# Kernel optimization log

Measured on AMD Instinct MI355X. Metric: run time of the kernel, lower is better.

## Reference

```python
import jax, jax.numpy as jnp
import numpy as np

B, T, E = 2, 2048, 768
H = 12
HD = E // H          # 64
ROT = 32             # rotary dim (= head_dim // 2 in CLVP)
SCALE = HD ** -0.5


def rotate_half(x):
    # split last dim into (2, d/2), rotate second half by 90 deg
    x = x.reshape(*x.shape[:-1], 2, x.shape[-1] // 2)
    x1, x2 = x[..., 0, :], x[..., 1, :]
    return jnp.concatenate([-x2, x1], axis=-1)


def apply_rotary_pos_emb(state, freqs):
    # state: (B*H, T, HD); freqs: (1, T, ROT)
    pos_emb_len = freqs.shape[-1]
    s_l, s_r = state[..., :pos_emb_len], state[..., pos_emb_len:]
    f = freqs[:, :, -s_l.shape[-1]:]
    s_l = s_l * jnp.cos(f) + rotate_half(s_l) * jnp.sin(f)
    return jnp.concatenate([s_l, s_r], axis=-1)


def setup_inputs() -> dict:
    key = jax.random.key(0)
    ks = jax.random.split(key, 6)
    hidden_states = jax.random.normal(ks[0], (B, T, E), dtype=jnp.float32)
    rotary_pos_emb = jax.random.uniform(ks[1], (1, T, ROT), dtype=jnp.float32)
    Wq = jax.random.normal(ks[2], (E, E), dtype=jnp.float32) * 0.02
    Wk = jax.random.normal(ks[3], (E, E), dtype=jnp.float32) * 0.02
    Wv = jax.random.normal(ks[4], (E, E), dtype=jnp.float32) * 0.02
    Wo = jax.random.normal(ks[5], (E, E), dtype=jnp.float32) * 0.02
    bo = jnp.zeros((E,), dtype=jnp.float32)
    return {"hidden_states": hidden_states, "rotary_pos_emb": rotary_pos_emb,
            "Wq": Wq, "Wk": Wk, "Wv": Wv, "Wo": Wo, "bo": bo}


def _shape(x):
    # (B, T, E) -> (B*H, T, HD)
    return x.reshape(B, T, H, HD).transpose(0, 2, 1, 3).reshape(B * H, T, HD)


def reference(hidden_states, rotary_pos_emb, Wq, Wk, Wv, Wo, bo):
    # nn.Linear: x @ W.T
    q = _shape(hidden_states @ Wq.T * SCALE)
    k = _shape(hidden_states @ Wk.T)
    v = _shape(hidden_states @ Wv.T)

    q = apply_rotary_pos_emb(q, rotary_pos_emb)
    k = apply_rotary_pos_emb(k, rotary_pos_emb)
    v = apply_rotary_pos_emb(v, rotary_pos_emb)  # CLVP applies RoPE to V too

    attn = jax.nn.softmax(jnp.einsum('bqd,bkd->bqk', q, k), axis=-1)  # (B*H, T, T)
    out = jnp.einsum('bqk,bkd->bqd', attn, v)                          # (B*H, T, HD)
    out = out.reshape(B, H, T, HD).transpose(0, 2, 1, 3).reshape(B, T, E)
    return out @ Wo.T + bo
```

## Files before the change

### kernel.cpp

```cpp
#include <hip/hip_runtime.h>
#include <hip/hip_bf16.h>

typedef unsigned short ushort_t;
typedef __attribute__((ext_vector_type(8))) short short8;
typedef __attribute__((ext_vector_type(4))) float f32x4;

constexpr int B  = 2;
constexpr int T  = 2048;
constexpr int E  = 768;
constexpr int H  = 12;
constexpr int HD = 64;
constexpr float QSCALE = 0.125f;

__device__ __forceinline__ ushort_t f2bf(float x) {
  unsigned int u = __float_as_uint(x);
  u += 0x7fffu + ((u >> 16) & 1u);
  return (ushort_t)(u >> 16);
}

__device__ __forceinline__ unsigned int pack_bf2(float a, float b) {
  __hip_bfloat162 h = __float22bfloat162_rn(float2{a, b});
  return *(unsigned int*)&h;
}

__device__ __forceinline__ int swz(int row, int col) {
  return row * 64 + ((((col >> 3) ^ (row & 7)) << 3) | (col & 7));
}

__device__ __forceinline__ void gl_lds16(const ushort_t* g, ushort_t* l) {
  __builtin_amdgcn_global_load_lds(
      (const __attribute__((address_space(1))) unsigned int*)g,
      (__attribute__((address_space(3))) unsigned int*)l, 16, 0, 0);
}

__global__ __launch_bounds__(256) void cvt_all(
    const float* __restrict__ X,  const float* __restrict__ Wq,
    const float* __restrict__ Wk, const float* __restrict__ Wv,
    const float* __restrict__ Wo, const float* __restrict__ rope,
    ushort_t* __restrict__ Xb,  ushort_t* __restrict__ Wqb,
    ushort_t* __restrict__ Wkb, ushort_t* __restrict__ Wvb,
    ushort_t* __restrict__ Wob, float* __restrict__ ct, float* __restrict__ st)
{
  constexpr int NX4 = (B * T * E) / 4;
  constexpr int NW4 = (E * E) / 4;
  constexpr int NC4 = NX4 + 4 * NW4;
  int i = blockIdx.x * 256 + threadIdx.x;
  if (i < NC4) {
    const float* s; ushort_t* d; int j;
    if (i < NX4) { s = X; d = Xb; j = i; }
    else {
      int t = i - NX4;
      int w = t / NW4; j = t - w * NW4;
      s = (w == 0) ? Wq : (w == 1) ? Wk : (w == 2) ? Wv : Wo;
      d = (w == 0) ? Wqb : (w == 1) ? Wkb : (w == 2) ? Wvb : Wob;
    }
    float4 v = ((const float4*)s)[j];
    ushort4 o;
    o.x = f2bf(v.x); o.y = f2bf(v.y); o.z = f2bf(v.z); o.w = f2bf(v.w);
    ((ushort4*)d)[j] = o;
  } else {
    int j = (i - NC4) * 4;
    float4 f = *(const float4*)(rope + j);
    float c, s;
    sincosf(f.x, &s, &c); ct[j+0] = c; st[j+0] = s;
    sincosf(f.y, &s, &c); ct[j+1] = c; st[j+1] = s;
    sincosf(f.z, &s, &c); ct[j+2] = c; st[j+2] = s;
    sincosf(f.w, &s, &c); ct[j+3] = c; st[j+3] = s;
  }
}

__global__ __launch_bounds__(256) void qkv_gemm(
    const ushort_t* __restrict__ Xb,
    const ushort_t* __restrict__ Wqb, const ushort_t* __restrict__ Wkb,
    const ushort_t* __restrict__ Wvb,
    const float* __restrict__ ct, const float* __restrict__ st,
    ushort_t* __restrict__ qfb, ushort_t* __restrict__ kfb, ushort_t* __restrict__ vfb)
{
  __shared__ __align__(16) ushort_t smem[128 * 64 + 3 * 64 * 64];
  ushort_t* Xs = smem;
  ushort_t* Ws[3] = { smem + 8192, smem + 8192 + 4096, smem + 8192 + 8192 };
  const int tid  = threadIdx.x;
  const int wave = tid >> 6;
  const int lane = tid & 63;
  const int l15  = lane & 15, quad = lane >> 4;
  const int h  = blockIdx.x;
  const int n0 = h * 64;
  const int m0 = blockIdx.y * 128;
  const ushort_t* Wsrc[3] = { Wqb, Wkb, Wvb };

  f32x4 acc[3][2][4];
  #pragma unroll
  for (int z = 0; z < 3; ++z)
    #pragma unroll
    for (int i = 0; i < 2; ++i)
      #pragma unroll
      for (int j = 0; j < 4; ++j) acc[z][i][j] = (f32x4){0.f, 0.f, 0.f, 0.f};

  const int li8 = lane >> 3, lc8 = lane & 7;
  const ushort_t* gX[4]; ushort_t* lX[4];
  #pragma unroll
  for (int j = 0; j < 4; ++j) {
    int row = wave * 32 + j * 8 + li8;
    int c = lc8 ^ (row & 7);
    gX[j] = Xb + (size_t)(m0 + row) * E + c * 8;
    lX[j] = Xs + (wave * 32 + j * 8) * 64;
  }
  const ushort_t* gW[3][2]; ushort_t* lW[3][2];
  #pragma unroll
  for (int z = 0; z < 3; ++z)
    #pragma unroll
    for (int j = 0; j < 2; ++j) {
      int row = wave * 16 + j * 8 + li8;
      int c = lc8 ^ (row & 7);
      gW[z][j] = Wsrc[z] + (size_t)(n0 + row) * E + c * 8;
      lW[z][j] = Ws[z] + (wave * 16 + j * 8) * 64;
    }

  for (int k0 = 0; k0 < E; k0 += 64) {
    #pragma unroll
    for (int j = 0; j < 4; ++j) gl_lds16(gX[j] + k0, lX[j]);
    #pragma unroll
    for (int z = 0; z < 3; ++z)
      #pragma unroll
      for (int j = 0; j < 2; ++j) gl_lds16(gW[z][j] + k0, lW[z][j]);
    __syncthreads();
    short8 a[2][2];
    #pragma unroll
    for (int mt = 0; mt < 2; ++mt)
      #pragma unroll
      for (int kh = 0; kh < 2; ++kh)
        a[mt][kh] = *(const short8*)&Xs[swz(wave * 32 + mt * 16 + l15, kh * 32 + quad * 8)];
    #pragma unroll
    for (int z = 0; z < 3; ++z)
      #pragma unroll
      for (int nt = 0; nt < 4; ++nt)
        #pragma unroll
        for (int kh = 0; kh < 2; ++kh) {
          short8 bb = *(const short8*)&Ws[z][swz(nt * 16 + l15, kh * 32 + quad * 8)];
          #pragma unroll
          for (int mt = 0; mt < 2; ++mt)
            acc[z][mt][nt] = __builtin_amdgcn_mfma_f32_16x16x32_bf16(a[mt][kh], bb, acc[z][mt][nt], 0, 0, 0);
        }
    __syncthreads();
  }

  const int b  = m0 >> 11;
  const int t0 = m0 & (T - 1);
  const int bh = b * H + h;

  #pragma unroll
  for (int z = 0; z < 2; ++z) {
    const float sc = (z == 0) ? QSCALE : 1.0f;
    #pragma unroll
    for (int mt = 0; mt < 2; ++mt) {
      #pragma unroll
      for (int r = 0; r < 4; ++r) {
        int mloc = wave * 32 + mt * 16 + quad * 4 + r;
        int t = (m0 + mloc) & (T - 1);
        float s0 = acc[z][mt][0][r] * sc;
        float s1 = acc[z][mt][1][r] * sc;
        float c0v = ct[t * 32 + l15],      sn0 = st[t * 32 + l15];
        float c1v = ct[t * 32 + 16 + l15], sn1 = st[t * 32 + 16 + l15];
        smem[swz(mloc, l15)]      = f2bf(s0 * c0v - s1 * sn0);
        smem[swz(mloc, 16 + l15)] = f2bf(s1 * c1v + s0 * sn1);
        smem[swz(mloc, 32 + l15)] = f2bf(acc[z][mt][2][r] * sc);
        smem[swz(mloc, 48 + l15)] = f2bf(acc[z][mt][3][r] * sc);
      }
    }
    __syncthreads();
    if (z == 0) {
      #pragma unroll
      for (int i = 0; i < 4; ++i) {
        int p = tid + 256 * i;
        int qtl = p >> 7, kh = (p >> 6) & 1, ln = p & 63;
        int tl = qtl * 16 + (ln & 15);
        int d  = kh * 32 + (ln >> 4) * 8;
        uint4 v = *(const uint4*)&smem[swz(tl, d)];
        size_t off = ((size_t)((bh * 128 + (t0 >> 4) + qtl) * 2 + kh)) * 512 + ln * 8;
        *(uint4*)(qfb + off) = v;
      }
    } else {
      #pragma unroll
      for (int i = 0; i < 4; ++i) {
        int p = tid + 256 * i;
        int ktl = p >> 9, mt = (p >> 7) & 3, kh = (p >> 6) & 1, ln = p & 63;
        int tl = ktl * 64 + mt * 16 + (ln & 15);
        int d  = kh * 32 + (ln >> 4) * 8;
        uint4 v = *(const uint4*)&smem[swz(tl, d)];
        size_t off = ((size_t)(((bh * 32 + (t0 >> 6) + ktl) * 4 + mt) * 2 + kh)) * 512 + ln * 8;
        *(uint4*)(kfb + off) = v;
      }
    }
    __syncthreads();
  }

  #pragma unroll
  for (int mt = 0; mt < 2; ++mt) {
    #pragma unroll
    for (int r = 0; r < 4; ++r) {
      int mloc = wave * 32 + mt * 16 + quad * 4 + r;
      int t = (m0 + mloc) & (T - 1);
      float s0 = acc[2][mt][0][r], s1 = acc[2][mt][1][r];
      float c0v = ct[t * 32 + l15],      sn0 = st[t * 32 + l15];
      float c1v = ct[t * 32 + 16 + l15], sn1 = st[t * 32 + 16 + l15];
      smem[(l15)      * 132 + mloc] = f2bf(s0 * c0v - s1 * sn0);
      smem[(16 + l15) * 132 + mloc] = f2bf(s1 * c1v + s0 * sn1);
      smem[(32 + l15) * 132 + mloc] = f2bf(acc[2][mt][2][r]);
      smem[(48 + l15) * 132 + mloc] = f2bf(acc[2][mt][3][r]);
    }
  }
  __syncthreads();
  #pragma unroll
  for (int i = 0; i < 4; ++i) {
    int p = tid + 256 * i;
    int ktl = p >> 9, nt = (p >> 7) & 3, kh = (p >> 6) & 1, ln = p & 63;
    int d  = nt * 16 + (ln & 15);
    int tl = ktl * 64 + kh * 32 + (ln >> 4) * 8;
    uint4 v = *(const uint4*)&smem[d * 132 + tl];
    size_t off = ((size_t)(((bh * 32 + (t0 >> 6) + ktl) * 4 + nt) * 2 + kh)) * 512 + ln * 8;
    *(uint4*)(vfb + off) = v;
  }
}

__global__ __launch_bounds__(256) void attn_kernel(
    const ushort_t* __restrict__ qfb, const ushort_t* __restrict__ kfb,
    const ushort_t* __restrict__ vfb, ushort_t* __restrict__ cbuf)
{
  __shared__ __align__(16) ushort_t Ps[4][32 * 40];
  __shared__ __align__(16) float Osh[2][32][66];
  __shared__ float Lsh[2][32];
  const int tid  = threadIdx.x;
  const int wave = tid >> 6;
  const int wq = wave >> 1, wk = wave & 1;
  const int lane = tid & 63;
  const int l15  = lane & 15, quad = lane >> 4;
  const int q0 = blockIdx.x * 64;
  const int bh = blockIdx.y;
  const ushort_t* Qf = qfb + (size_t)bh * (T * HD);
  const ushort_t* Kf = kfb + (size_t)bh * (T * HD);
  const ushort_t* Vf = vfb + (size_t)bh * (T * HD);
  ushort_t* Pw = &Ps[wave][0];

  short8 qa[2][2];
  #pragma unroll
  for (int qg = 0; qg < 2; ++qg)
    #pragma unroll
    for (int kh = 0; kh < 2; ++kh)
      qa[qg][kh] = *(const short8*)(Qf + ((size_t)(((q0 >> 4) + wq * 2 + qg) * 2 + kh)) * 512 + lane * 8);

  short8 ka[2][2], va[4];
  #pragma unroll
  for (int i = 0; i < 2; ++i)
    #pragma unroll
    for (int kh = 0; kh < 2; ++kh)
      ka[i][kh] = *(const short8*)(Kf + ((size_t)((wk * 2 + i) * 2 + kh)) * 512 + lane * 8);
  #pragma unroll
  for (int nt = 0; nt < 4; ++nt)
    va[nt] = *(const short8*)(Vf + ((size_t)(nt * 2 + wk)) * 512 + lane * 8);

  f32x4 o[2][4];
  #pragma unroll
  for (int qg = 0; qg < 2; ++qg)
    #pragma unroll
    for (int nt = 0; nt < 4; ++nt) o[qg][nt] = (f32x4){0.f, 0.f, 0.f, 0.f};
  float lsum[2] = {0.f, 0.f};

  for (int kt = 0; kt < T / 64; ++kt) {
    const int ktn = (kt + 1 < T / 64) ? kt + 1 : kt;
    short8 kn[2][2], vn[4];
    #pragma unroll
    for (int i = 0; i < 2; ++i)
      #pragma unroll
      for (int kh = 0; kh < 2; ++kh)
        kn[i][kh] = *(const short8*)(Kf + ((size_t)((ktn * 4 + wk * 2 + i) * 2 + kh)) * 512 + lane * 8);
    #pragma unroll
    for (int nt = 0; nt < 4; ++nt)
      vn[nt] = *(const short8*)(Vf + ((size_t)((ktn * 4 + nt) * 2 + wk)) * 512 + lane * 8);

    f32x4 ss[2][2];
    #pragma unroll
    for (int mt = 0; mt < 2; ++mt)
      #pragma unroll
      for (int qg = 0; qg < 2; ++qg) {
        ss[mt][qg] = (f32x4){0.f, 0.f, 0.f, 0.f};
        ss[mt][qg] = __builtin_amdgcn_mfma_f32_16x16x32_bf16(ka[mt][0], qa[qg][0], ss[mt][qg], 0, 0, 0);
        ss[mt][qg] = __builtin_amdgcn_mfma_f32_16x16x32_bf16(ka[mt][1], qa[qg][1], ss[mt][qg], 0, 0, 0);
      }

    #pragma unroll
    for (int qg = 0; qg < 2; ++qg) {
      #pragma unroll
      for (int mt = 0; mt < 2; ++mt) {
        float p0 = __expf(ss[mt][qg][0]);
        float p1 = __expf(ss[mt][qg][1]);
        float p2 = __expf(ss[mt][qg][2]);
        float p3 = __expf(ss[mt][qg][3]);
        lsum[qg] += (p0 + p1) + (p2 + p3);
        uint2 w2;
        w2.x = pack_bf2(p0, p1);
        w2.y = pack_bf2(p2, p3);
        *(uint2*)&Pw[(qg * 16 + l15) * 40 + mt * 16 + quad * 4] = w2;
      }
    }

    short8 pa0 = *(const short8*)&Pw[(l15) * 40 + quad * 8];
    short8 pa1 = *(const short8*)&Pw[(16 + l15) * 40 + quad * 8];
    #pragma unroll
    for (int nt = 0; nt < 4; ++nt) {
      o[0][nt] = __builtin_amdgcn_mfma_f32_16x16x32_bf16(pa0, va[nt], o[0][nt], 0, 0, 0);
      o[1][nt] = __builtin_amdgcn_mfma_f32_16x16x32_bf16(pa1, va[nt], o[1][nt], 0, 0, 0);
    }

    #pragma unroll
    for (int i = 0; i < 2; ++i) {
      ka[i][0] = kn[i][0];
      ka[i][1] = kn[i][1];
    }
    #pragma unroll
    for (int nt = 0; nt < 4; ++nt) va[nt] = vn[nt];
  }

  #pragma unroll
  for (int qg = 0; qg < 2; ++qg) {
    lsum[qg] += __shfl_xor(lsum[qg], 16);
    lsum[qg] += __shfl_xor(lsum[qg], 32);
  }

  if (wk == 0) {
    #pragma unroll
    for (int qg = 0; qg < 2; ++qg)
      #pragma unroll
      for (int nt = 0; nt < 4; ++nt)
        #pragma unroll
        for (int r = 0; r < 4; ++r)
          Osh[wq][qg * 16 + quad * 4 + r][nt * 16 + l15] = o[qg][nt][r];
    if (lane < 16) {
      Lsh[wq][l15]      = lsum[0];
      Lsh[wq][16 + l15] = lsum[1];
    }
  }
  __syncthreads();
  if (wk == 1) {
    const int b = bh / H, h = bh % H;
    #pragma unroll
    for (int qg = 0; qg < 2; ++qg) {
      float ltot = lsum[qg] + Lsh[wq][qg * 16 + l15];
      float inv0 = 1.0f / ltot;
      #pragma unroll
      for (int r = 0; r < 4; ++r) {
        float inv = __shfl(inv0, quad * 4 + r);
        int t = q0 + wq * 32 + qg * 16 + quad * 4 + r;
        size_t base = ((size_t)b * T + t) * E + h * HD;
        #pragma unroll
        for (int nt = 0; nt < 4; ++nt) {
          float v = o[qg][nt][r] + Osh[wq][qg * 16 + quad * 4 + r][nt * 16 + l15];
          cbuf[base + nt * 16 + l15] = f2bf(v * inv);
        }
      }
    }
  }
}

__global__ __launch_bounds__(256) void out_gemm(
    const ushort_t* __restrict__ Xc, const ushort_t* __restrict__ Wob,
    const float* __restrict__ bo, float* __restrict__ out)
{
  __shared__ __align__(16) ushort_t Xs[128 * 64];
  __shared__ __align__(16) ushort_t Ws[64 * 64];
  const int tid  = threadIdx.x;
  const int wave = tid >> 6;
  const int lane = tid & 63;
  const int l15  = lane & 15, quad = lane >> 4;
  const int n0 = blockIdx.x * 64;
  const int m0 = blockIdx.y * 128;

  f32x4 acc[2][4];
  #pragma unroll
  for (int i = 0; i < 2; ++i)
    #pragma unroll
    for (int j = 0; j < 4; ++j) acc[i][j] = (f32x4){0.f, 0.f, 0.f, 0.f};

  const int li8 = lane >> 3, lc8 = lane & 7;
  const ushort_t* gX[4]; ushort_t* lX[4];
  #pragma unroll
  for (int j = 0; j < 4; ++j) {
    int row = wave * 32 + j * 8 + li8;
    int c = lc8 ^ (row & 7);
    gX[j] = Xc + (size_t)(m0 + row) * E + c * 8;
    lX[j] = Xs + (wave * 32 + j * 8) * 64;
  }
  const ushort_t* gW[2]; ushort_t* lW[2];
  #pragma unroll
  for (int j = 0; j < 2; ++j) {
    int row = wave * 16 + j * 8 + li8;
    int c = lc8 ^ (row & 7);
    gW[j] = Wob + (size_t)(n0 + row) * E + c * 8;
    lW[j] = Ws + (wave * 16 + j * 8) * 64;
  }

  for (int k0 = 0; k0 < E; k0 += 64) {
    #pragma unroll
    for (int j = 0; j < 4; ++j) gl_lds16(gX[j] + k0, lX[j]);
    #pragma unroll
    for (int j = 0; j < 2; ++j) gl_lds16(gW[j] + k0, lW[j]);
    __syncthreads();
    short8 a[2][2];
    #pragma unroll
    for (int mt = 0; mt < 2; ++mt)
      #pragma unroll
      for (int kh = 0; kh < 2; ++kh)
        a[mt][kh] = *(const short8*)&Xs[swz(wave * 32 + mt * 16 + l15, kh * 32 + quad * 8)];
    #pragma unroll
    for (int nt = 0; nt < 4; ++nt) {
      #pragma unroll
      for (int kh = 0; kh < 2; ++kh) {
        short8 bb = *(const short8*)&Ws[swz(nt * 16 + l15, kh * 32 + quad * 8)];
        #pragma unroll
        for (int mt = 0; mt < 2; ++mt)
          acc[mt][nt] = __builtin_amdgcn_mfma_f32_16x16x32_bf16(a[mt][kh], bb, acc[mt][nt], 0, 0, 0);
      }
    }
    __syncthreads();
  }

  float bias[4];
  #pragma unroll
  for (int nt = 0; nt < 4; ++nt) bias[nt] = bo[n0 + nt * 16 + l15];
  #pragma unroll
  for (int mt = 0; mt < 2; ++mt) {
    #pragma unroll
    for (int r = 0; r < 4; ++r) {
      int m = m0 + wave * 32 + mt * 16 + quad * 4 + r;
      float* op = out + (size_t)m * E + n0;
      op[l15]      = acc[mt][0][r] + bias[0];
      op[16 + l15] = acc[mt][1][r] + bias[1];
      op[32 + l15] = acc[mt][2][r] + bias[2];
      op[48 + l15] = acc[mt][3][r] + bias[3];
    }
  }
}

extern "C" void kernel_launch(void* const* d_in, const int* in_sizes, int n_in,
                              void* d_out, int out_size, void* d_ws, size_t ws_size,
                              hipStream_t stream) {
  (void)in_sizes; (void)n_in; (void)out_size; (void)ws_size;
  const float* X    = (const float*)d_in[0];
  const float* rope = (const float*)d_in[1];
  const float* Wq   = (const float*)d_in[2];
  const float* Wk   = (const float*)d_in[3];
  const float* Wv   = (const float*)d_in[4];
  const float* Wo   = (const float*)d_in[5];
  const float* bo   = (const float*)d_in[6];
  float* out = (float*)d_out;

  const size_t NX = (size_t)B * T * E;
  const size_t NW = (size_t)E * E;
  const size_t NR = (size_t)T * 32;
  ushort_t* Xb  = (ushort_t*)d_ws;
  ushort_t* Wqb = Xb  + NX;
  ushort_t* Wkb = Wqb + NW;
  ushort_t* Wvb = Wkb + NW;
  ushort_t* Wob = Wvb + NW;
  ushort_t* qfb = Wob + NW;
  ushort_t* kfb = qfb + NX;
  ushort_t* vfb = kfb + NX;
  ushort_t* cb  = vfb + NX;
  float* ct = (float*)(cb + NX);
  float* st = ct + NR;

  const int total4 = (int)((NX + 4 * NW + NR) / 4);
  cvt_all<<<total4 / 256, 256, 0, stream>>>(X, Wq, Wk, Wv, Wo, rope,
                                            Xb, Wqb, Wkb, Wvb, Wob, ct, st);

  qkv_gemm<<<dim3(H, (B * T) / 128), 256, 0, stream>>>(
      Xb, Wqb, Wkb, Wvb, ct, st, qfb, kfb, vfb);
  attn_kernel<<<dim3(T / 64, B * H), 256, 0, stream>>>(qfb, kfb, vfb, cb);
  out_gemm<<<dim3(E / 64, (B * T) / 128), 256, 0, stream>>>(cb, Wob, bo, out);
}
```

Baseline: 162.6 us.

## Double-buffer LDS in projection GEMMs and compute softmax row sums via MFMA

The QKV and output GEMMs now use two LDS buffers and issue the next k-tile's global-to-LDS loads before computing on the current tile, removing one barrier per iteration so load latency can overlap with MFMA work. The attention kernel drops per-element scalar row-sum accumulation and the shuffle reduction, and instead multiplies the P tile by a ones vector with an extra MFMA per query group. Doubling LDS may reduce occupancy. The async loads into the next buffer rely on the trailing barrier plus the compiler's vmcnt waiting before the next read, which is a correctness risk.

Result: faster. 158.3 us (-2.7%).

```diff
diff --git a/kernel.cpp b/kernel.cpp
--- a/kernel.cpp
+++ b/kernel.cpp
@@ -76,9 +76,7 @@
     const float* __restrict__ ct, const float* __restrict__ st,
     ushort_t* __restrict__ qfb, ushort_t* __restrict__ kfb, ushort_t* __restrict__ vfb)
 {
-  __shared__ __align__(16) ushort_t smem[128 * 64 + 3 * 64 * 64];
-  ushort_t* Xs = smem;
-  ushort_t* Ws[3] = { smem + 8192, smem + 8192 + 4096, smem + 8192 + 8192 };
+  __shared__ __align__(16) ushort_t smem[2 * 20480];
   const int tid  = threadIdx.x;
   const int wave = tid >> 6;
   const int lane = tid & 63;
@@ -97,15 +95,15 @@
       for (int j = 0; j < 4; ++j) acc[z][i][j] = (f32x4){0.f, 0.f, 0.f, 0.f};
 
   const int li8 = lane >> 3, lc8 = lane & 7;
-  const ushort_t* gX[4]; ushort_t* lX[4];
+  const ushort_t* gX[4]; int lXo[4];
   #pragma unroll
   for (int j = 0; j < 4; ++j) {
     int row = wave * 32 + j * 8 + li8;
     int c = lc8 ^ (row & 7);
     gX[j] = Xb + (size_t)(m0 + row) * E + c * 8;
-    lX[j] = Xs + (wave * 32 + j * 8) * 64;
-  }
-  const ushort_t* gW[3][2]; ushort_t* lW[3][2];
+    lXo[j] = (wave * 32 + j * 8) * 64;
+  }
+  const ushort_t* gW[3][2]; int lWo[3][2];
   #pragma unroll
   for (int z = 0; z < 3; ++z)
     #pragma unroll
@@ -113,17 +111,29 @@
       int row = wave * 16 + j * 8 + li8;
       int c = lc8 ^ (row & 7);
       gW[z][j] = Wsrc[z] + (size_t)(n0 + row) * E + c * 8;
-      lW[z][j] = Ws[z] + (wave * 16 + j * 8) * 64;
-    }
+      lWo[z][j] = 8192 + z * 4096 + (wave * 16 + j * 8) * 64;
+    }
+
+  #pragma unroll
+  for (int j = 0; j < 4; ++j) gl_lds16(gX[j], smem + lXo[j]);
+  #pragma unroll
+  for (int z = 0; z < 3; ++z)
+    #pragma unroll
+    for (int j = 0; j < 2; ++j) gl_lds16(gW[z][j], smem + lWo[z][j]);
+  __syncthreads();
 
   for (int k0 = 0; k0 < E; k0 += 64) {
-    #pragma unroll
-    for (int j = 0; j < 4; ++j) gl_lds16(gX[j] + k0, lX[j]);
-    #pragma unroll
-    for (int z = 0; z < 3; ++z)
-      #pragma unroll
-      for (int j = 0; j < 2; ++j) gl_lds16(gW[z][j] + k0, lW[z][j]);
-    __syncthreads();
+    const int cur = (k0 >> 6) & 1;
+    const int nxt = cur ^ 1;
+    if (k0 + 64 < E) {
+      #pragma unroll
+      for (int j = 0; j < 4; ++j) gl_lds16(gX[j] + k0 + 64, smem + nxt * 20480 + lXo[j]);
+      #pragma unroll
+      for (int z = 0; z < 3; ++z)
+        #pragma unroll
+        for (int j = 0; j < 2; ++j) gl_lds16(gW[z][j] + k0 + 64, smem + nxt * 20480 + lWo[z][j]);
+    }
+    const ushort_t* Xs = smem + cur * 20480;
     short8 a[2][2];
     #pragma unroll
     for (int mt = 0; mt < 2; ++mt)
@@ -131,16 +141,18 @@
       for (int kh = 0; kh < 2; ++kh)
         a[mt][kh] = *(const short8*)&Xs[swz(wave * 32 + mt * 16 + l15, kh * 32 + quad * 8)];
     #pragma unroll
-    for (int z = 0; z < 3; ++z)
+    for (int z = 0; z < 3; ++z) {
+      const ushort_t* Wz = smem + cur * 20480 + 8192 + z * 4096;
       #pragma unroll
       for (int nt = 0; nt < 4; ++nt)
         #pragma unroll
         for (int kh = 0; kh < 2; ++kh) {
-          short8 bb = *(const short8*)&Ws[z][swz(nt * 16 + l15, kh * 32 + quad * 8)];
+          short8 bb = *(const short8*)&Wz[swz(nt * 16 + l15, kh * 32 + quad * 8)];
           #pragma unroll
           for (int mt = 0; mt < 2; ++mt)
             acc[z][mt][nt] = __builtin_amdgcn_mfma_f32_16x16x32_bf16(a[mt][kh], bb, acc[z][mt][nt], 0, 0, 0);
         }
+    }
     __syncthreads();
   }
 
@@ -241,6 +253,9 @@
   const ushort_t* Vf = vfb + (size_t)bh * (T * HD);
   ushort_t* Pw = &Ps[wave][0];
 
+  const short8 ones8 = {(short)0x3F80, (short)0x3F80, (short)0x3F80, (short)0x3F80,
+                        (short)0x3F80, (short)0x3F80, (short)0x3F80, (short)0x3F80};
+
   short8 qa[2][2];
   #pragma unroll
   for (int qg = 0; qg < 2; ++qg)
@@ -258,12 +273,13 @@
   for (int nt = 0; nt < 4; ++nt)
     va[nt] = *(const short8*)(Vf + ((size_t)(nt * 2 + wk)) * 512 + lane * 8);
 
-  f32x4 o[2][4];
-  #pragma unroll
-  for (int qg = 0; qg < 2; ++qg)
+  f32x4 o[2][4], osum[2];
+  #pragma unroll
+  for (int qg = 0; qg < 2; ++qg) {
     #pragma unroll
     for (int nt = 0; nt < 4; ++nt) o[qg][nt] = (f32x4){0.f, 0.f, 0.f, 0.f};
-  float lsum[2] = {0.f, 0.f};
+    osum[qg] = (f32x4){0.f, 0.f, 0.f, 0.f};
+  }
 
   for (int kt = 0; kt < T / 64; ++kt) {
     const int ktn = (kt + 1 < T / 64) ? kt + 1 : kt;
@@ -295,7 +311,6 @@
         float p1 = __expf(ss[mt][qg][1]);
         float p2 = __expf(ss[mt][qg][2]);
         float p3 = __expf(ss[mt][qg][3]);
-        lsum[qg] += (p0 + p1) + (p2 + p3);
         uint2 w2;
         w2.x = pack_bf2(p0, p1);
         w2.y = pack_bf2(p2, p3);
@@ -305,6 +320,8 @@
 
     short8 pa0 = *(const short8*)&Pw[(l15) * 40 + quad * 8];
     short8 pa1 = *(const short8*)&Pw[(16 + l15) * 40 + quad * 8];
+    osum[0] = __builtin_amdgcn_mfma_f32_16x16x32_bf16(pa0, ones8, osum[0], 0, 0, 0);
+    osum[1] = __builtin_amdgcn_mfma_f32_16x16x32_bf16(pa1, ones8, osum[1], 0, 0, 0);
     #pragma unroll
     for (int nt = 0; nt < 4; ++nt) {
       o[0][nt] = __builtin_amdgcn_mfma_f32_16x16x32_bf16(pa0, va[nt], o[0][nt], 0, 0, 0);
@@ -320,23 +337,19 @@
     for (int nt = 0; nt < 4; ++nt) va[nt] = vn[nt];
   }
 
-  #pragma unroll
-  for (int qg = 0; qg < 2; ++qg) {
-    lsum[qg] += __shfl_xor(lsum[qg], 16);
-    lsum[qg] += __shfl_xor(lsum[qg], 32);
-  }
-
   if (wk == 0) {
     #pragma unroll
-    for (int qg = 0; qg < 2; ++qg)
+    for (int qg = 0; qg < 2; ++qg) {
       #pragma unroll
       for (int nt = 0; nt < 4; ++nt)
         #pragma unroll
         for (int r = 0; r < 4; ++r)
           Osh[wq][qg * 16 + quad * 4 + r][nt * 16 + l15] = o[qg][nt][r];
-    if (lane < 16) {
-      Lsh[wq][l15]      = lsum[0];
-      Lsh[wq][16 + l15] = lsum[1];
+      if (l15 == 0) {
+        #pragma unroll
+        for (int r = 0; r < 4; ++r)
+          Lsh[wq][qg * 16 + quad * 4 + r] = osum[qg][r];
+      }
     }
   }
   __syncthreads();
@@ -344,11 +357,10 @@
     const int b = bh / H, h = bh % H;
     #pragma unroll
     for (int qg = 0; qg < 2; ++qg) {
-      float ltot = lsum[qg] + Lsh[wq][qg * 16 + l15];
-      float inv0 = 1.0f / ltot;
       #pragma unroll
       for (int r = 0; r < 4; ++r) {
-        float inv = __shfl(inv0, quad * 4 + r);
+        float ltot = osum[qg][r] + Lsh[wq][qg * 16 + quad * 4 + r];
+        float inv = 1.0f / ltot;
         int t = q0 + wq * 32 + qg * 16 + quad * 4 + r;
         size_t base = ((size_t)b * T + t) * E + h * HD;
         #pragma unroll
@@ -365,8 +377,7 @@
     const ushort_t* __restrict__ Xc, const ushort_t* __restrict__ Wob,
     const float* __restrict__ bo, float* __restrict__ out)
 {
-  __shared__ __align__(16) ushort_t Xs[128 * 64];
-  __shared__ __align__(16) ushort_t Ws[64 * 64];
+  __shared__ __align__(16) ushort_t smem[2 * 12288];
   const int tid  = threadIdx.x;
   const int wave = tid >> 6;
   const int lane = tid & 63;
@@ -381,29 +392,40 @@
     for (int j = 0; j < 4; ++j) acc[i][j] = (f32x4){0.f, 0.f, 0.f, 0.f};
 
   const int li8 = lane >> 3, lc8 = lane & 7;
-  const ushort_t* gX[4]; ushort_t* lX[4];
+  const ushort_t* gX[4]; int lXo[4];
   #pragma unroll
   for (int j = 0; j < 4; ++j) {
     int row = wave * 32 + j * 8 + li8;
     int c = lc8 ^ (row & 7);
     gX[j] = Xc + (size_t)(m0 + row) * E + c * 8;
-    lX[j] = Xs + (wave * 32 + j * 8) * 64;
-  }
-  const ushort_t* gW[2]; ushort_t* lW[2];
+    lXo[j] = (wave * 32 + j * 8) * 64;
+  }
+  const ushort_t* gW[2]; int lWo[2];
   #pragma unroll
   for (int j = 0; j < 2; ++j) {
     int row = wave * 16 + j * 8 + li8;
     int c = lc8 ^ (row & 7);
     gW[j] = Wob + (size_t)(n0 + row) * E + c * 8;
-    lW[j] = Ws + (wave * 16 + j * 8) * 64;
-  }
+    lWo[j] = 8192 + (wave * 16 + j * 8) * 64;
+  }
+
+  #pragma unroll
+  for (int j = 0; j < 4; ++j) gl_lds16(gX[j], smem + lXo[j]);
+  #pragma unroll
+  for (int j = 0; j < 2; ++j) gl_lds16(gW[j], smem + lWo[j]);
+  __syncthreads();
 
   for (int k0 = 0; k0 < E; k0 += 64) {
-    #pragma unroll
-    for (int j = 0; j < 4; ++j) gl_lds16(gX[j] + k0, lX[j]);
-    #pragma unroll
-    for (int j = 0; j < 2; ++j) gl_lds16(gW[j] + k0, lW[j]);
-    __syncthreads();
+    const int cur = (k0 >> 6) & 1;
+    const int nxt = cur ^ 1;
+    if (k0 + 64 < E) {
+      #pragma unroll
+      for (int j = 0; j < 4; ++j) gl_lds16(gX[j] + k0 + 64, smem + nxt * 12288 + lXo[j]);
+      #pragma unroll
+      for (int j = 0; j < 2; ++j) gl_lds16(gW[j] + k0 + 64, smem + nxt * 12288 + lWo[j]);
+    }
+    const ushort_t* Xs = smem + cur * 12288;
+    const ushort_t* Ws = smem + cur * 12288 + 8192;
     short8 a[2][2];
     #pragma unroll
     for (int mt = 0; mt < 2; ++mt)
```
